# Kernel optimization log

Measured on AMD Instinct MI355X. Metric: run time of the kernel, lower is better.

## Reference

```python
import jax, jax.numpy as jnp
import numpy as np

B, S, D, H = 2, 2048, 1024, 16
HD = D // H  # head_dim = 64
ROPE_BASE = 10000.0


def apply_rope(x, positions):
    # x: [B, S, H, HD], positions: [B, S] int. Rotate-half RoPE.
    d = x.shape[-1]
    inv_freq = 1.0 / (ROPE_BASE ** (jnp.arange(0, d, 2, dtype=jnp.float32) / d))  # [d/2]
    ang = positions[..., None].astype(jnp.float32) * inv_freq  # [B, S, d/2]
    cos = jnp.cos(ang)[:, :, None, :]
    sin = jnp.sin(ang)[:, :, None, :]
    x1, x2 = jnp.split(x, 2, axis=-1)
    return jnp.concatenate([x1 * cos - x2 * sin, x2 * cos + x1 * sin], axis=-1).astype(x.dtype)


def setup_inputs() -> dict:
    key = jax.random.key(0)
    k1, k2, k3 = jax.random.split(key, 3)
    inputs = jax.random.normal(k1, (B, S, D), dtype=jnp.float32)
    # nn.Linear weights [out_features, in_features]
    W_in = jax.random.normal(k2, (3 * D, D), dtype=jnp.float32) * (1.0 / np.sqrt(D))
    W_out = jax.random.normal(k3, (D, D), dtype=jnp.float32) * (1.0 / np.sqrt(D))
    positions = jnp.tile(jnp.arange(S, dtype=jnp.int32)[None, :], (B, 1))  # [B, S]
    return {"inputs": inputs, "positions": positions, "W_in": W_in, "W_out": W_out}


def reference(inputs, positions, W_in, W_out):
    # fused QKV projection: [B, S, 3D], head-major layout per rearrange '(heads qkv)'
    qkv = jnp.einsum('bsd,ed->bse', inputs, W_in)
    qkv = qkv.reshape(B, S, H, 3 * HD)
    q, k, v = jnp.split(qkv, 3, axis=-1)  # each [B, S, H, HD]
    q = apply_rope(q, positions)
    k = apply_rope(k, positions)
    # einsum_attention (inference path): scale query, full masked softmax
    q = q / jnp.sqrt(jnp.asarray(HD, dtype=q.dtype))
    scores = jnp.einsum('bqhd,bkhd->bhqk', q, k)  # [B, H, S, S]
    mask = (jnp.arange(S)[None, None, :] <= positions[:, :, None])[:, None, :, :]  # [B,1,S,S]
    big_neg = jnp.finfo(scores.dtype).min
    scores = jnp.where(mask, scores, big_neg)
    attn = jax.nn.softmax(scores, axis=-1)
    x = jnp.einsum('bhqk,bkhd->bqhd', attn, v).reshape(B, S, D)
    return jnp.einsum('bsd,ed->bse', x, W_out)
```

## Files before the change

### kernel.cpp

```cpp
#include <hip/hip_runtime.h>
#include <stdint.h>
#include <math.h>

#define B_ 2
#define S_ 2048
#define D_ 1024
#define H_ 16
#define HD_ 64
#define KVBLK 64

typedef __bf16 bf16_t;
typedef __bf16 bf16x4 __attribute__((ext_vector_type(4)));
typedef __bf16 bf16x8 __attribute__((ext_vector_type(8)));
typedef float f32x4 __attribute__((ext_vector_type(4)));
typedef float f32x16 __attribute__((ext_vector_type(16)));
typedef float float4v __attribute__((ext_vector_type(4)));

#define L2E 1.4426950408889634f
#define NINF (-__builtin_inff())

__device__ __forceinline__ void gload_lds16(const bf16_t* g, bf16_t* l) {
  __builtin_amdgcn_global_load_lds((const __attribute__((address_space(1))) void*)g,
                                   (__attribute__((address_space(3))) void*)l, 16, 0, 0);
}

__device__ __forceinline__ uint32_t packbf(float a, float b) {
  union { __bf16 h[2]; uint32_t u; } cvt;
  cvt.h[0] = (__bf16)a; cvt.h[1] = (__bf16)b;
  return cvt.u;
}

__global__ void cast_bf16_kernel(const float* __restrict__ src, bf16_t* __restrict__ dst, int n4) {
  int i = blockIdx.x * blockDim.x + threadIdx.x;
  int stride = gridDim.x * blockDim.x;
  for (; i < n4; i += stride) {
    float4v f = *(const float4v*)(src + (size_t)i * 4);
    bf16x4 o;
    o[0] = (__bf16)f[0]; o[1] = (__bf16)f[1]; o[2] = (__bf16)f[2]; o[3] = (__bf16)f[3];
    *(bf16x4*)(dst + (size_t)i * 4) = o;
  }
}

template <typename OutT>
__global__ __launch_bounds__(256) void gemm_bt(const bf16_t* __restrict__ A,
                                               const bf16_t* __restrict__ Bm,
                                               OutT* __restrict__ C,
                                               int M, int N, int K) {
  __shared__ bf16_t As[128 * 32];
  __shared__ bf16_t Bs[128 * 32];
  const int t = threadIdx.x;
  const int lane = t & 63, wave = t >> 6;
  const int wr = wave >> 1, wc = wave & 1;
  const int qr = lane & 15, g = lane >> 4;
  const int bm = blockIdx.x, bn = blockIdx.y;

  f32x4 acc[4][4];
#pragma unroll
  for (int m = 0; m < 4; m++)
#pragma unroll
    for (int n = 0; n < 4; n++) acc[m][n] = (f32x4){0.f, 0.f, 0.f, 0.f};

  const bf16_t* Abase = A + (size_t)(bm * 128) * K;
  const bf16_t* Bbase = Bm + (size_t)(bn * 128) * K;
  const int srow = t >> 2;
  const int scol = (t & 3) * 8;

  for (int kk = 0; kk < K; kk += 32) {
    gload_lds16(Abase + (size_t)srow * K + kk + scol,        As + t * 8);
    gload_lds16(Abase + (size_t)(srow + 64) * K + kk + scol, As + 2048 + t * 8);
    gload_lds16(Bbase + (size_t)srow * K + kk + scol,        Bs + t * 8);
    gload_lds16(Bbase + (size_t)(srow + 64) * K + kk + scol, Bs + 2048 + t * 8);
    __syncthreads();
    bf16x8 a[4], b[4];
#pragma unroll
    for (int m = 0; m < 4; m++)
      a[m] = *(const bf16x8*)(As + (wr * 64 + m * 16 + qr) * 32 + g * 8);
#pragma unroll
    for (int n = 0; n < 4; n++)
      b[n] = *(const bf16x8*)(Bs + (wc * 64 + n * 16 + qr) * 32 + g * 8);
#pragma unroll
    for (int m = 0; m < 4; m++)
#pragma unroll
      for (int n = 0; n < 4; n++)
        acc[m][n] = __builtin_amdgcn_mfma_f32_16x16x32_bf16(a[m], b[n], acc[m][n], 0, 0, 0);
    __syncthreads();
  }

#pragma unroll
  for (int m = 0; m < 4; m++) {
    int row0 = bm * 128 + wr * 64 + m * 16 + g * 4;
#pragma unroll
    for (int n = 0; n < 4; n++) {
      int col = bn * 128 + wc * 64 + n * 16 + qr;
#pragma unroll
      for (int r = 0; r < 4; r++)
        C[(size_t)(row0 + r) * N + col] = (OutT)acc[m][n][r];
    }
  }
}

__global__ void rope_qk_kernel(const bf16_t* __restrict__ qkv, const int* __restrict__ pos,
                               bf16_t* __restrict__ Q, bf16_t* __restrict__ Ko) {
  int idx = blockIdx.x * blockDim.x + threadIdx.x;
  if (idx >= B_ * S_ * H_ * 32) return;
  int i = idx & 31;
  int h = (idx >> 5) & (H_ - 1);
  int bs = idx >> 9;
  const bf16_t* row = qkv + (size_t)bs * (3 * D_) + h * 192;
  float q1 = (float)row[i], q2 = (float)row[i + 32];
  float k1 = (float)row[64 + i], k2 = (float)row[96 + i];
  int p = pos[bs];
  float inv = exp2f(-(float)i * (13.287712379549449f / 32.0f));
  float ang = (float)p * inv;
  float sn, cs;
  sincosf(ang, &sn, &cs);
  float qo1 = (q1 * cs - q2 * sn) * 0.125f;
  float qo2 = (q2 * cs + q1 * sn) * 0.125f;
  float ko1 = k1 * cs - k2 * sn;
  float ko2 = k2 * cs + k1 * sn;
  int b = bs >> 11, s = bs & (S_ - 1);
  size_t o = ((size_t)(b * H_ + h) * S_ + s) * HD_ + i;
  Q[o] = (__bf16)qo1;  Q[o + 32] = (__bf16)qo2;
  Ko[o] = (__bf16)ko1; Ko[o + 32] = (__bf16)ko2;
}

__global__ __launch_bounds__(256) void v_transpose_kernel(const bf16_t* __restrict__ qkv,
                                                          bf16_t* __restrict__ Vt) {
  __shared__ bf16_t tile[64][72];
  int t = threadIdx.x;
  int s0 = blockIdx.x * 64;
  int h = blockIdx.y, b = blockIdx.z;
  int sl = t >> 4;
  int cb = (t & 15) * 4;
#pragma unroll
  for (int it = 0; it < 4; it++) {
    int s = sl + it * 16;
    const bf16_t* src = qkv + (size_t)(b * S_ + s0 + s) * (3 * D_) + h * 192 + 128 + cb;
    bf16x4 v = *(const bf16x4*)src;
    tile[cb + 0][s] = v[0]; tile[cb + 1][s] = v[1];
    tile[cb + 2][s] = v[2]; tile[cb + 3][s] = v[3];
  }
  __syncthreads();
#pragma unroll
  for (int it = 0; it < 4; it++) {
    int d = sl + it * 16;
    bf16x4 v;
    v[0] = tile[d][cb]; v[1] = tile[d][cb + 1]; v[2] = tile[d][cb + 2]; v[3] = tile[d][cb + 3];
    *(bf16x4*)(Vt + ((size_t)((b * H_ + h) * HD_ + d)) * S_ + s0 + cb) = v;
  }
}

__global__ __launch_bounds__(256) void attn_kernel(const bf16_t* __restrict__ Q,
                                                   const bf16_t* __restrict__ K,
                                                   const bf16_t* __restrict__ Vt,
                                                   const int* __restrict__ pos,
                                                   bf16_t* __restrict__ O) {
  __shared__ bf16_t Ks[2][64 * 64];
  __shared__ bf16_t Vs[2][64 * 64];

  const int t = threadIdx.x;
  const int lane = t & 63, wv = t >> 6;
  const int l31 = lane & 31, hi = lane >> 5;

  const int bid = blockIdx.x;
  const int bh = (bid & 7) * 4 + ((bid >> 3) & 3);
  const int qblk = 15 - (bid >> 5);
  const int b = bh >> 4, h = bh & 15;
  const int q0 = qblk * 128;

  const bf16_t* Qb = Q + (size_t)bh * (S_ * HD_);
  const bf16_t* Kb = K + (size_t)bh * (S_ * HD_);
  const bf16_t* Vb = Vt + (size_t)bh * (HD_ * S_);

  const int qrow = q0 + wv * 32 + l31;
  bf16x8 qf[4];
#pragma unroll
  for (int c = 0; c < 4; c++)
    qf[c] = *(const bf16x8*)(Qb + (size_t)qrow * HD_ + c * 16 + hi * 8);

  const int prow = pos[b * S_ + qrow];
  int wmin = prow;
#pragma unroll
  for (int off = 1; off < 32; off <<= 1) wmin = min(wmin, __shfl_xor(wmin, off));

  int mp = max(pos[b * S_ + q0 + lane], pos[b * S_ + q0 + 64 + lane]);
#pragma unroll
  for (int off = 1; off < 64; off <<= 1) mp = max(mp, __shfl_xor(mp, off));
  const int ntiles = min(S_ / KVBLK, (mp >> 6) + 1);

  const int r0 = t >> 3, c0 = t & 7;
  const int r1 = (t + 256) >> 3, c1 = t & 7;
  const bf16_t* KgA = Kb + (size_t)r0 * HD_ + ((c0 ^ (r0 & 7)) * 8);
  const bf16_t* KgB = Kb + (size_t)r1 * HD_ + ((c1 ^ (r1 & 7)) * 8);
  const bf16_t* VgA = Vb + (size_t)r0 * S_ + ((c0 ^ (r0 & 7)) * 8);
  const bf16_t* VgB = Vb + (size_t)r1 * S_ + ((c1 ^ (r1 & 7)) * 8);
  const int ldsA = t * 8, ldsB = (t + 256) * 8;

  f32x16 oT[2];
#pragma unroll
  for (int dt = 0; dt < 2; dt++)
#pragma unroll
    for (int r = 0; r < 16; r++) oT[dt][r] = 0.f;
  float m_run = NINF, l_run = 0.f;

  gload_lds16(KgA, Ks[0] + ldsA);
  gload_lds16(KgB, Ks[0] + ldsB);
  gload_lds16(VgA, Vs[0] + ldsA);
  gload_lds16(VgB, Vs[0] + ldsB);
  __syncthreads();

  for (int kt = 0; kt < ntiles; ++kt) {
    const int k0 = kt * KVBLK;
    const int cur = kt & 1;
    if (kt + 1 < ntiles) {
      const int kn = (kt + 1) * KVBLK;
      gload_lds16(KgA + (size_t)kn * HD_, Ks[cur ^ 1] + ldsA);
      gload_lds16(KgB + (size_t)kn * HD_, Ks[cur ^ 1] + ldsB);
      gload_lds16(VgA + kn, Vs[cur ^ 1] + ldsA);
      gload_lds16(VgB + kn, Vs[cur ^ 1] + ldsB);
    }
    const bf16_t* Kc = Ks[cur];
    const bf16_t* Vc = Vs[cur];

    f32x16 s0, s1;
#pragma unroll
    for (int r = 0; r < 16; r++) { s0[r] = 0.f; s1[r] = 0.f; }
    __builtin_amdgcn_s_setprio(1);
#pragma unroll
    for (int c = 0; c < 4; c++) {
      const int c2 = c * 2 + hi;
      const int kr0 = l31;
      const int kr1 = 32 + l31;
      bf16x8 kf0 = *(const bf16x8*)(Kc + kr0 * 64 + ((c2 ^ (kr0 & 7)) * 8));
      bf16x8 kf1 = *(const bf16x8*)(Kc + kr1 * 64 + ((c2 ^ (kr1 & 7)) * 8));
      s0 = __builtin_amdgcn_mfma_f32_32x32x16_bf16(kf0, qf[c], s0, 0, 0, 0);
      s1 = __builtin_amdgcn_mfma_f32_32x32x16_bf16(kf1, qf[c], s1, 0, 0, 0);
    }
    __builtin_amdgcn_s_setprio(0);

    float p0[16], p1[16];
    if (k0 + 63 > wmin) {
#pragma unroll
      for (int r = 0; r < 16; r++) {
        int koff = (r & 3) + 8 * (r >> 2) + 4 * hi;
        p0[r] = (k0 + koff <= prow) ? s0[r] : NINF;
        p1[r] = (k0 + 32 + koff <= prow) ? s1[r] : NINF;
      }
    } else {
#pragma unroll
      for (int r = 0; r < 16; r++) { p0[r] = s0[r]; p1[r] = s1[r]; }
    }

    float tm = NINF;
#pragma unroll
    for (int r = 0; r < 16; r++) tm = fmaxf(tm, fmaxf(p0[r], p1[r]));
    tm = fmaxf(tm, __shfl_xor(tm, 32));
    if (__any(tm > m_run + 8.0f)) {
      float mn = fmaxf(fmaxf(m_run, tm), -1e30f);
      float scale = exp2f((m_run - mn) * L2E);
      l_run *= scale;
#pragma unroll
      for (int dt = 0; dt < 2; dt++)
#pragma unroll
        for (int r = 0; r < 16; r++) oT[dt][r] *= scale;
      m_run = mn;
    }
    const float mnl = m_run * L2E;
    float rs = 0.f;
#pragma unroll
    for (int r = 0; r < 16; r++) {
      p0[r] = exp2f(p0[r] * L2E - mnl);
      p1[r] = exp2f(p1[r] * L2E - mnl);
      rs += p0[r] + p1[r];
    }
    rs += __shfl_xor(rs, 32);
    l_run += rs;

#pragma unroll
    for (int kc = 0; kc < 4; kc++) {
      const float* P = (kc < 2) ? p0 : p1;
      const int rb = (kc & 1) * 8;
      uint32_t xa0 = packbf(P[rb + 0], P[rb + 1]);
      uint32_t xa1 = packbf(P[rb + 2], P[rb + 3]);
      uint32_t xb0 = packbf(P[rb + 4], P[rb + 5]);
      uint32_t xb1 = packbf(P[rb + 6], P[rb + 7]);
      uint32_t sa0 = (uint32_t)__shfl_xor((int)xa0, 32);
      uint32_t sa1 = (uint32_t)__shfl_xor((int)xa1, 32);
      uint32_t sb0 = (uint32_t)__shfl_xor((int)xb0, 32);
      uint32_t sb1 = (uint32_t)__shfl_xor((int)xb1, 32);
      union { uint32_t u[4]; bf16x8 v; } pf;
      pf.u[0] = hi ? sb0 : xa0;
      pf.u[1] = hi ? sb1 : xa1;
      pf.u[2] = hi ? xb0 : sa0;
      pf.u[3] = hi ? xb1 : sa1;
      __builtin_amdgcn_s_setprio(1);
#pragma unroll
      for (int dt = 0; dt < 2; dt++) {
        const int vr = dt * 32 + l31;
        const int c2 = kc * 2 + hi;
        bf16x8 vf = *(const bf16x8*)(Vc + vr * 64 + ((c2 ^ (vr & 7)) * 8));
        oT[dt] = __builtin_amdgcn_mfma_f32_32x32x16_bf16(vf, pf.v, oT[dt], 0, 0, 0);
      }
      __builtin_amdgcn_s_setprio(0);
    }

    __syncthreads();
  }

  const float rl = (l_run > 0.f) ? 1.0f / l_run : 0.f;
  bf16_t* Ot = (bf16_t*)Ks + wv * 2048;
#pragma unroll
  for (int dt = 0; dt < 2; dt++)
#pragma unroll
    for (int r = 0; r < 16; r++) {
      int chunk = dt * 4 + (r >> 2);
      int el = (r & 3) + 4 * hi;
      Ot[l31 * 64 + ((chunk ^ (l31 & 7)) * 8) + el] = (__bf16)(oT[dt][r] * rl);
    }
  __syncthreads();
#pragma unroll
  for (int it = 0; it < 4; it++) {
    int qr2 = (lane >> 3) + it * 8;
    int cc = lane & 7;
    bf16x8 v = *(const bf16x8*)(Ot + qr2 * 64 + ((cc ^ (qr2 & 7)) * 8));
    *(bf16x8*)(&O[(size_t)(b * S_ + q0 + wv * 32 + qr2) * D_ + h * 64 + cc * 8]) = v;
  }
}

extern "C" void kernel_launch(void* const* d_in, const int* in_sizes, int n_in,
                              void* d_out, int out_size, void* d_ws, size_t ws_size,
                              hipStream_t stream) {
  const float* inputs = (const float*)d_in[0];
  const int* positions = (const int*)d_in[1];
  const float* W_in = (const float*)d_in[2];
  const float* W_out = (const float*)d_in[3];
  float* out = (float*)d_out;

  bf16_t* X_bf = (bf16_t*)d_ws;
  bf16_t* Win_bf = X_bf + (size_t)4096 * 1024;
  bf16_t* Wout_bf = Win_bf + (size_t)3072 * 1024;
  bf16_t* qkv_bf = Wout_bf + (size_t)1024 * 1024;
  bf16_t* Qb = qkv_bf + (size_t)4096 * 3072;
  bf16_t* Kb = Qb + (size_t)B_ * H_ * S_ * HD_;
  bf16_t* Vtb = Kb + (size_t)B_ * H_ * S_ * HD_;
  bf16_t* Ob = Vtb + (size_t)B_ * H_ * S_ * HD_;

  cast_bf16_kernel<<<dim3(2048), dim3(256), 0, stream>>>(inputs, X_bf, (4096 * 1024) / 4);
  cast_bf16_kernel<<<dim3(2048), dim3(256), 0, stream>>>(W_in, Win_bf, (3072 * 1024) / 4);
  cast_bf16_kernel<<<dim3(1024), dim3(256), 0, stream>>>(W_out, Wout_bf, (1024 * 1024) / 4);

  gemm_bt<bf16_t><<<dim3(32, 24), dim3(256), 0, stream>>>(X_bf, Win_bf, qkv_bf, 4096, 3072, 1024);

  rope_qk_kernel<<<dim3((B_ * S_ * H_ * 32) / 256), dim3(256), 0, stream>>>(qkv_bf, positions, Qb, Kb);
  v_transpose_kernel<<<dim3(S_ / 64, H_, B_), dim3(256), 0, stream>>>(qkv_bf, Vtb);

  attn_kernel<<<dim3(512), dim3(256), 0, stream>>>(Qb, Kb, Vtb, positions, Ob);

  gemm_bt<float><<<dim3(32, 8), dim3(256), 0, stream>>>(Ob, Wout_bf, out, 4096, 1024, 1024);
}
```

Baseline: 161.7 us.

## Add 256x256 pipelined QKV GEMM with swizzled LDS and interleaved prefetch

```diff
diff --git a/kernel.cpp b/kernel.cpp
--- a/kernel.cpp
+++ b/kernel.cpp
@@ -92,6 +92,163 @@
 #pragma unroll
     for (int n = 0; n < 4; n++) {
       int col = bn * 128 + wc * 64 + n * 16 + qr;
+#pragma unroll
+      for (int r = 0; r < 4; r++)
+        C[(size_t)(row0 + r) * N + col] = (OutT)acc[m][n][r];
+    }
+  }
+}
+
+template <typename OutT>
+__global__ __launch_bounds__(512, 2) void gemm256(const bf16_t* __restrict__ A,
+                                                  const bf16_t* __restrict__ Bm,
+                                                  OutT* __restrict__ C,
+                                                  int M, int N, int K) {
+  __shared__ bf16_t As[2][256 * 64];
+  __shared__ bf16_t Bs[2][256 * 64];
+  const int t = threadIdx.x;
+  const int lane = t & 63, wid = t >> 6;
+  const int qr = lane & 15, g = lane >> 4;
+  const int wm = wid >> 2, wn = wid & 3;
+  const int bm = blockIdx.x, bn = blockIdx.y;
+  const int NT = K >> 6;
+
+  const bf16_t* Ab = A + (size_t)(bm * 256) * K;
+  const bf16_t* Bb = Bm + (size_t)(bn * 256) * K;
+
+  const bf16_t* srcA[4];
+  const bf16_t* srcB[4];
+  int ldsOff[4];
+#pragma unroll
+  for (int i = 0; i < 4; i++) {
+    int e = t + 512 * i;
+    int row = e >> 3, cs = e & 7;
+    int gcol = (cs ^ (row & 7)) * 8;
+    srcA[i] = Ab + (size_t)row * K + gcol;
+    srcB[i] = Bb + (size_t)row * K + gcol;
+    ldsOff[i] = e * 8;
+  }
+
+  f32x4 acc[8][4];
+#pragma unroll
+  for (int m = 0; m < 8; m++)
+#pragma unroll
+    for (int n = 0; n < 4; n++) acc[m][n] = (f32x4){0.f, 0.f, 0.f, 0.f};
+
+#define RD(buf_, r_, k_) (*(const bf16x8*)((buf_) + (r_) * 64 + ((((k_) * 4 + g) ^ ((r_) & 7)) * 8)))
+
+#pragma unroll
+  for (int i = 0; i < 4; i++) gload_lds16(srcA[i], As[0] + ldsOff[i]);
+#pragma unroll
+  for (int i = 0; i < 4; i++) gload_lds16(srcB[i], Bs[0] + ldsOff[i]);
+#pragma unroll
+  for (int i = 0; i < 4; i++) gload_lds16(srcA[i] + 64, As[1] + ldsOff[i]);
+#pragma unroll
+  for (int i = 0; i < 4; i++) gload_lds16(srcB[i] + 64, Bs[1] + ldsOff[i]);
+
+  for (int T = 0; T < NT; ++T) {
+    bf16_t* A_c = As[T & 1];
+    bf16_t* B_c = Bs[T & 1];
+    if (T + 1 < NT) asm volatile("s_waitcnt vmcnt(8)" ::: "memory");
+    else            asm volatile("s_waitcnt vmcnt(0)" ::: "memory");
+    __builtin_amdgcn_sched_barrier(0);
+    __builtin_amdgcn_s_barrier();
+
+    const bool st = (T + 2 < NT);
+    const int kt2 = (T + 2) * 64;
+
+    bf16x8 alo[4][2], ahi[4][2], bfr[4][2];
+
+#pragma unroll
+    for (int m = 0; m < 4; m++) {
+      int r = wm * 128 + m * 16 + qr;
+      alo[m][0] = RD(A_c, r, 0); alo[m][1] = RD(A_c, r, 1);
+    }
+#pragma unroll
+    for (int n = 0; n < 2; n++) {
+      int r = wn * 64 + n * 16 + qr;
+      bfr[n][0] = RD(B_c, r, 0); bfr[n][1] = RD(B_c, r, 1);
+    }
+    __builtin_amdgcn_s_barrier();
+    __builtin_amdgcn_s_setprio(1);
+#pragma unroll
+    for (int m = 0; m < 4; m++)
+#pragma unroll
+      for (int n = 0; n < 2; n++)
+#pragma unroll
+        for (int k = 0; k < 2; k++)
+          acc[m][n] = __builtin_amdgcn_mfma_f32_16x16x32_bf16(alo[m][k], bfr[n][k], acc[m][n], 0, 0, 0);
+    __builtin_amdgcn_s_setprio(0);
+    __builtin_amdgcn_s_barrier();
+
+#pragma unroll
+    for (int n = 2; n < 4; n++) {
+      int r = wn * 64 + n * 16 + qr;
+      bfr[n][0] = RD(B_c, r, 0); bfr[n][1] = RD(B_c, r, 1);
+    }
+    if (st) {
+      gload_lds16(srcA[0] + kt2, A_c + ldsOff[0]);
+      gload_lds16(srcA[2] + kt2, A_c + ldsOff[2]);
+    }
+    __builtin_amdgcn_s_barrier();
+    __builtin_amdgcn_s_setprio(1);
+#pragma unroll
+    for (int m = 0; m < 4; m++)
+#pragma unroll
+      for (int n = 2; n < 4; n++)
+#pragma unroll
+        for (int k = 0; k < 2; k++)
+          acc[m][n] = __builtin_amdgcn_mfma_f32_16x16x32_bf16(alo[m][k], bfr[n][k], acc[m][n], 0, 0, 0);
+    __builtin_amdgcn_s_setprio(0);
+    __builtin_amdgcn_s_barrier();
+
+#pragma unroll
+    for (int m = 0; m < 4; m++) {
+      int r = wm * 128 + (m + 4) * 16 + qr;
+      ahi[m][0] = RD(A_c, r, 0); ahi[m][1] = RD(A_c, r, 1);
+    }
+    if (st) {
+      gload_lds16(srcB[0] + kt2, B_c + ldsOff[0]);
+      gload_lds16(srcB[1] + kt2, B_c + ldsOff[1]);
+      gload_lds16(srcB[2] + kt2, B_c + ldsOff[2]);
+      gload_lds16(srcB[3] + kt2, B_c + ldsOff[3]);
+    }
+    __builtin_amdgcn_s_barrier();
+    __builtin_amdgcn_s_setprio(1);
+#pragma unroll
+    for (int m = 0; m < 4; m++)
+#pragma unroll
+      for (int n = 0; n < 2; n++)
+#pragma unroll
+        for (int k = 0; k < 2; k++)
+          acc[m + 4][n] = __builtin_amdgcn_mfma_f32_16x16x32_bf16(ahi[m][k], bfr[n][k], acc[m + 4][n], 0, 0, 0);
+    __builtin_amdgcn_s_setprio(0);
+    __builtin_amdgcn_s_barrier();
+
+    if (st) {
+      gload_lds16(srcA[1] + kt2, A_c + ldsOff[1]);
+      gload_lds16(srcA[3] + kt2, A_c + ldsOff[3]);
+    }
+    __builtin_amdgcn_s_barrier();
+    __builtin_amdgcn_s_setprio(1);
+#pragma unroll
+    for (int m = 0; m < 4; m++)
+#pragma unroll
+      for (int n = 2; n < 4; n++)
+#pragma unroll
+        for (int k = 0; k < 2; k++)
+          acc[m + 4][n] = __builtin_amdgcn_mfma_f32_16x16x32_bf16(ahi[m][k], bfr[n][k], acc[m + 4][n], 0, 0, 0);
+    __builtin_amdgcn_s_setprio(0);
+    __builtin_amdgcn_s_barrier();
+  }
+#undef RD
+
+#pragma unroll
+  for (int m = 0; m < 8; m++) {
+    int row0 = bm * 256 + wm * 128 + m * 16 + g * 4;
+#pragma unroll
+    for (int n = 0; n < 4; n++) {
+      int col = bn * 256 + wn * 64 + n * 16 + qr;
 #pragma unroll
       for (int r = 0; r < 4; r++)
         C[(size_t)(row0 + r) * N + col] = (OutT)acc[m][n][r];
@@ -349,7 +506,7 @@
   cast_bf16_kernel<<<dim3(2048), dim3(256), 0, stream>>>(W_in, Win_bf, (3072 * 1024) / 4);
   cast_bf16_kernel<<<dim3(1024), dim3(256), 0, stream>>>(W_out, Wout_bf, (1024 * 1024) / 4);
 
-  gemm_bt<bf16_t><<<dim3(32, 24), dim3(256), 0, stream>>>(X_bf, Win_bf, qkv_bf, 4096, 3072, 1024);
+  gemm256<bf16_t><<<dim3(16, 12), dim3(512), 0, stream>>>(X_bf, Win_bf, qkv_bf, 4096, 3072, 1024);
 
   rope_qk_kernel<<<dim3((B_ * S_ * H_ * 32) / 256), dim3(256), 0, stream>>>(qkv_bf, positions, Qb, Kb);
   v_transpose_kernel<<<dim3(S_ / 64, H_, B_), dim3(256), 0, stream>>>(qkv_bf, Vtb);
```

New measurement: 160.1 us. About the same (-1.0%).
